# Kernel optimization log

Hardware: AMD Instinct MI355X
Metric: run time of the kernel (lower is better)

## Reference

```python
import jax, jax.numpy as jnp
import numpy as np
import math

HIDDEN = 2048
N_HEADS = 32
N_KV_HEADS = 8
HEAD_DIM = HIDDEN // N_HEADS
KV_REPEATS = N_HEADS // N_KV_HEADS
INTER = 4 * HIDDEN
EPS = 1e-5
B, Q, K = 2, 2048, 2048


def setup_inputs() -> dict:
    key = jax.random.key(0)
    ks = jax.random.split(key, 10)
    s = 0.02
    return {
        "hidden_states": jax.random.normal(ks[0], (B, Q, HIDDEN), jnp.float32),
        "key_states": jax.random.normal(ks[1], (B, K, N_KV_HEADS, HEAD_DIM), jnp.float32),
        "value_states": jax.random.normal(ks[2], (B, K, N_KV_HEADS, HEAD_DIM), jnp.float32),
        "gmu_memory": jnp.zeros((1,), jnp.float32),
        "w_ln1": jnp.ones((HIDDEN,), jnp.float32),
        "w_ln2": jnp.ones((HIDDEN,), jnp.float32),
        "w_q": jax.random.normal(ks[3], (N_HEADS * HEAD_DIM, HIDDEN), jnp.float32) * s,
        "w_o": jax.random.normal(ks[4], (HIDDEN, N_HEADS * HEAD_DIM), jnp.float32) * s,
        "w_gate": jax.random.normal(ks[5], (INTER, HIDDEN), jnp.float32) * s,
        "w_up": jax.random.normal(ks[6], (INTER, HIDDEN), jnp.float32) * s,
        "w_down": jax.random.normal(ks[7], (HIDDEN, INTER), jnp.float32) * s,
        "cu_seqlens_q": jnp.array([0, 1024, 2048], jnp.int32),
        "cu_seqlens_k": jnp.array([0, 1024, 2048], jnp.int32),
    }


def _rms_norm(x, w, eps=EPS):
    var = jnp.mean(jnp.square(x), axis=-1, keepdims=True)
    return (x * jax.lax.rsqrt(var + eps)) * w


def _segment_ids(cu, length):
    # position p belongs to segment i iff cu[i] <= p < cu[i+1]
    return jnp.searchsorted(cu[1:], jnp.arange(length), side="right")


def _attn_mask(q_len, k_len, cu_q, cu_k, causal=True, window_size=None):
    seg_q = _segment_ids(cu_q, q_len)  # [Q]
    seg_k = _segment_ids(cu_k, k_len)  # [K]
    mask = seg_q[:, None] == seg_k[None, :]
    if causal:
        q_pos = jnp.arange(q_len)[:, None]
        k_pos = jnp.arange(k_len)[None, :]
        offset = max(k_len - q_len, 0)
        mask = mask & (k_pos <= q_pos + offset)
    if window_size is not None and window_size > 0:
        q_pos = jnp.arange(q_len)[:, None] + max(k_len - q_len, 0)
        k_pos = jnp.arange(k_len)[None, :]
        mask = mask & (q_pos - k_pos < window_size)
    return mask  # [Q, K] bool


def reference(hidden_states, key_states, value_states, gmu_memory,
              w_ln1, w_ln2, w_q, w_o, w_gate, w_up, w_down,
              cu_seqlens_q, cu_seqlens_k):
    b, q_len, _ = hidden_states.shape
    residual = hidden_states
    normed = _rms_norm(hidden_states, w_ln1)

    # --- cross attention (shared KV, GQA) ---
    q = (normed @ w_q.T).reshape(b, q_len, N_HEADS, HEAD_DIM)
    k = jnp.repeat(key_states, KV_REPEATS, axis=2)    # [B,K,H,hd]
    v = jnp.repeat(value_states, KV_REPEATS, axis=2)  # [B,K,H,hd]
    k_len = k.shape[1]

    scores = jnp.einsum("bqhd,bkhd->bhqk", q, k) / math.sqrt(HEAD_DIM)
    mask = _attn_mask(q_len, k_len, cu_seqlens_q, cu_seqlens_k, causal=True)
    neg = jnp.finfo(scores.dtype).min
    scores = jnp.where(mask[None, None, :, :], scores, neg)
    probs = jax.nn.softmax(scores.astype(jnp.float32), axis=-1).astype(q.dtype)
    attn = jnp.einsum("bhqk,bkhd->bqhd", probs, v).reshape(b, q_len, -1)
    mixed = attn @ w_o.T

    hidden = residual + mixed

    # --- Llama MLP: down(silu(gate(x)) * up(x)) ---
    normed2 = _rms_norm(hidden, w_ln2)
    mlp = (jax.nn.silu(normed2 @ w_gate.T) * (normed2 @ w_up.T)) @ w_down.T
    return hidden + mlp
```

## Files before the change

### kernel.cpp

```cpp
#include <hip/hip_runtime.h>

typedef __bf16 bf16_t;
typedef bf16_t bf16x8 __attribute__((ext_vector_type(8)));
typedef float floatx4 __attribute__((ext_vector_type(4)));

#define HIDDEN 2048
#define NHEADS 32
#define NKV 8
#define HD 64
#define INTER 8192
#define SEQQ 2048
#define SEQK 2048
#define NBATCH 2
#define NEGBIG (-3.0e38f)

__device__ __forceinline__ floatx4 mfma16(bf16x8 a, bf16x8 b, floatx4 c) {
  return __builtin_amdgcn_mfma_f32_16x16x32_bf16(a, b, c, 0, 0, 0);
}

__device__ __forceinline__ uint4 pack8(const float* __restrict__ p) {
  float4 f0 = *(const float4*)p;
  float4 f1 = *(const float4*)(p + 4);
  union { uint4 u; bf16_t e[8]; } r;
  r.e[0] = (bf16_t)f0.x; r.e[1] = (bf16_t)f0.y; r.e[2] = (bf16_t)f0.z; r.e[3] = (bf16_t)f0.w;
  r.e[4] = (bf16_t)f1.x; r.e[5] = (bf16_t)f1.y; r.e[6] = (bf16_t)f1.z; r.e[7] = (bf16_t)f1.w;
  return r.u;
}

__global__ __launch_bounds__(256) void cvt_kernel(const float* __restrict__ src,
                                                  bf16_t* __restrict__ dst, int n8) {
  const int stride = gridDim.x * 256;
  for (int i = blockIdx.x * 256 + threadIdx.x; i < n8; i += stride)
    *(uint4*)(dst + (size_t)i * 8) = pack8(src + (size_t)i * 8);
}

__global__ __launch_bounds__(256) void rmsnorm_kernel(const float* __restrict__ x,
                                                      const float* __restrict__ w,
                                                      bf16_t* __restrict__ y) {
  const int row = blockIdx.x;
  const int tid = threadIdx.x;
  const float* xr = x + (size_t)row * HIDDEN + tid * 8;
  float4 x0 = *(const float4*)xr;
  float4 x1 = *(const float4*)(xr + 4);
  float xf[8] = {x0.x, x0.y, x0.z, x0.w, x1.x, x1.y, x1.z, x1.w};
  float ss = 0.f;
#pragma unroll
  for (int j = 0; j < 8; ++j) ss += xf[j] * xf[j];
#pragma unroll
  for (int off = 32; off >= 1; off >>= 1) ss += __shfl_xor(ss, off);
  __shared__ float red[4];
  if ((tid & 63) == 0) red[tid >> 6] = ss;
  __syncthreads();
  float tot = red[0] + red[1] + red[2] + red[3];
  float rs = 1.0f / sqrtf(tot / (float)HIDDEN + 1e-5f);
  const float* wr = w + tid * 8;
  float4 w0 = *(const float4*)wr;
  float4 w1 = *(const float4*)(wr + 4);
  float wf[8] = {w0.x, w0.y, w0.z, w0.w, w1.x, w1.y, w1.z, w1.w};
  bf16x8 ov;
#pragma unroll
  for (int j = 0; j < 8; ++j) ov[j] = (bf16_t)(xf[j] * rs * wf[j]);
  *(bf16x8*)(y + (size_t)row * HIDDEN + tid * 8) = ov;
}

template <int ROWS>
__device__ __forceinline__ void stage_tile(bf16_t* lds, const bf16_t* src, int ldK) {
  const int tid = (int)threadIdx.x;
  const int wid = tid >> 6;
  const int row0 = tid >> 3;
  const int scol = (((tid & 7) ^ (row0 & 7)) * 8);
#pragma unroll
  for (int i = 0; i < ROWS / 32; ++i) {
    const bf16_t* g = src + (size_t)(i * 32 + row0) * ldK + scol;
    __builtin_amdgcn_global_load_lds(
        (const __attribute__((address_space(1))) void*)g,
        (__attribute__((address_space(3))) void*)(lds + i * 2048 + wid * 512), 16, 0, 0);
  }
}

__device__ __forceinline__ bf16x8 ldfrag(const bf16_t* lds, int row, int kslot) {
  return *(const bf16x8*)(lds + row * 64 + ((kslot ^ (row & 7)) * 8));
}

template <int EPI, typename CT>
__global__ __launch_bounds__(256) void gemm_bt16(const bf16_t* __restrict__ A,
                                                 const bf16_t* __restrict__ W,
                                                 const float* __restrict__ resid,
                                                 CT* __restrict__ C, int Kd, int N) {
  const int m0 = blockIdx.y * 128, n0 = blockIdx.x * 128;
  const int tid = threadIdx.x;
  const int wid = tid >> 6, lane = tid & 63, quad = lane >> 4, l15 = lane & 15;
  const int wr = wid >> 1, wc = wid & 1;
  __shared__ __align__(16) bf16_t Asm[128 * 64];
  __shared__ __align__(16) bf16_t Bsm[128 * 64];
  floatx4 acc[4][4];
  floatx4 zero = {0.f, 0.f, 0.f, 0.f};
#pragma unroll
  for (int mi = 0; mi < 4; ++mi)
#pragma unroll
    for (int ni = 0; ni < 4; ++ni) acc[mi][ni] = zero;

  const bf16_t* Ab = A + (size_t)m0 * Kd;
  const bf16_t* Wb = W + (size_t)n0 * Kd;

  for (int kt = 0; kt < Kd; kt += 64) {
    __syncthreads();
    stage_tile<128>(Asm, Ab + kt, Kd);
    stage_tile<128>(Bsm, Wb + kt, Kd);
    __syncthreads();
#pragma unroll
    for (int kk = 0; kk < 2; ++kk) {
      const int ks = kk * 4 + quad;
      bf16x8 af[4], bfr[4];
#pragma unroll
      for (int mi = 0; mi < 4; ++mi) af[mi] = ldfrag(Asm, wr * 64 + mi * 16 + l15, ks);
#pragma unroll
      for (int ni = 0; ni < 4; ++ni) bfr[ni] = ldfrag(Bsm, wc * 64 + ni * 16 + l15, ks);
#pragma unroll
      for (int mi = 0; mi < 4; ++mi)
#pragma unroll
        for (int ni = 0; ni < 4; ++ni) acc[mi][ni] = mfma16(af[mi], bfr[ni], acc[mi][ni]);
    }
  }

#pragma unroll
  for (int mi = 0; mi < 4; ++mi) {
    const int mb = m0 + wr * 64 + mi * 16 + quad * 4;
#pragma unroll
    for (int ni = 0; ni < 4; ++ni) {
      const int n = n0 + wc * 64 + ni * 16 + l15;
      floatx4 v = acc[mi][ni];
#pragma unroll
      for (int r = 0; r < 4; ++r) {
        size_t idx = (size_t)(mb + r) * N + n;
        float val = v[r];
        if (EPI == 1) val += resid[idx];
        C[idx] = (CT)val;
      }
    }
  }
}

__global__ __launch_bounds__(256) void gateup16(const bf16_t* __restrict__ A,
                                                const bf16_t* __restrict__ Wg,
                                                const bf16_t* __restrict__ Wu,
                                                bf16_t* __restrict__ C, int Kd, int N) {
  const int m0 = blockIdx.y * 128, n0 = blockIdx.x * 64;
  const int tid = threadIdx.x;
  const int wid = tid >> 6, lane = tid & 63, quad = lane >> 4, l15 = lane & 15;
  const int wr = wid >> 1, wc = wid & 1;
  __shared__ __align__(16) bf16_t Asm[128 * 64];
  __shared__ __align__(16) bf16_t Gsm[64 * 64];
  __shared__ __align__(16) bf16_t Usm[64 * 64];
  floatx4 accg[4][2], accu[4][2];
  floatx4 zero = {0.f, 0.f, 0.f, 0.f};
#pragma unroll
  for (int mi = 0; mi < 4; ++mi)
#pragma unroll
    for (int ni = 0; ni < 2; ++ni) { accg[mi][ni] = zero; accu[mi][ni] = zero; }

  const bf16_t* Ab = A + (size_t)m0 * Kd;
  const bf16_t* Gb = Wg + (size_t)n0 * Kd;
  const bf16_t* Ub = Wu + (size_t)n0 * Kd;

  for (int kt = 0; kt < Kd; kt += 64) {
    __syncthreads();
    stage_tile<128>(Asm, Ab + kt, Kd);
    stage_tile<64>(Gsm, Gb + kt, Kd);
    stage_tile<64>(Usm, Ub + kt, Kd);
    __syncthreads();
#pragma unroll
    for (int kk = 0; kk < 2; ++kk) {
      const int ks = kk * 4 + quad;
      bf16x8 af[4];
#pragma unroll
      for (int mi = 0; mi < 4; ++mi) af[mi] = ldfrag(Asm, wr * 64 + mi * 16 + l15, ks);
#pragma unroll
      for (int ni = 0; ni < 2; ++ni) {
        bf16x8 bg = ldfrag(Gsm, wc * 32 + ni * 16 + l15, ks);
        bf16x8 bu = ldfrag(Usm, wc * 32 + ni * 16 + l15, ks);
#pragma unroll
        for (int mi = 0; mi < 4; ++mi) {
          accg[mi][ni] = mfma16(af[mi], bg, accg[mi][ni]);
          accu[mi][ni] = mfma16(af[mi], bu, accu[mi][ni]);
        }
      }
    }
  }

#pragma unroll
  for (int mi = 0; mi < 4; ++mi) {
    const int mb = m0 + wr * 64 + mi * 16 + quad * 4;
#pragma unroll
    for (int ni = 0; ni < 2; ++ni) {
      const int n = n0 + wc * 32 + ni * 16 + l15;
#pragma unroll
      for (int r = 0; r < 4; ++r) {
        float g = accg[mi][ni][r];
        float u = accu[mi][ni][r];
        float act = g / (1.f + __expf(-g)) * u;
        C[(size_t)(mb + r) * N + n] = (bf16_t)act;
      }
    }
  }
}

__global__ __launch_bounds__(256) void attn16(const bf16_t* __restrict__ qbuf,
                                              const bf16_t* __restrict__ kbuf,
                                              const bf16_t* __restrict__ vbuf,
                                              const int* __restrict__ cuq,
                                              const int* __restrict__ cuk,
                                              bf16_t* __restrict__ obuf) {
  const int qt = blockIdx.x, h = blockIdx.y, b = blockIdx.z;
  const int hk = h >> 2;
  const int tid = threadIdx.x;
  const int wid = tid >> 6, lane = tid & 63, quad = lane >> 4, l15 = lane & 15;
  __shared__ __align__(16) bf16_t Kt[64 * 72];
  __shared__ __align__(16) bf16_t Vt[64 * 72];
  __shared__ __align__(16) bf16_t Pt[64 * 72];
  const int cq1 = cuq[1], ck1 = cuk[1];

  const int qrow_a = qt * 64 + wid * 16 + l15;
  const bf16_t* qp = qbuf + ((size_t)(b * SEQQ + qrow_a)) * HIDDEN + h * HD;
  bf16x8 qf0 = *(const bf16x8*)(qp + quad * 8);
  bf16x8 qf1 = *(const bf16x8*)(qp + 32 + quad * 8);

  floatx4 Of[4];
  floatx4 zero = {0.f, 0.f, 0.f, 0.f};
#pragma unroll
  for (int df = 0; df < 4; ++df) Of[df] = zero;
  float m_r[4], l_r[4];
#pragma unroll
  for (int r = 0; r < 4; ++r) { m_r[r] = -1e30f; l_r[r] = 0.f; }
  const int q_row0 = qt * 64 + wid * 16 + quad * 4;
  int seg_q[4];
#pragma unroll
  for (int r = 0; r < 4; ++r) seg_q[r] = (q_row0 + r >= cq1) ? 1 : 0;
  const bool blk_seg1 = (qt * 64 >= cq1);

  const int stag_row = tid >> 3;
  const int stag_c = (tid & 7) * 8;
  const int kt_start = blk_seg1 ? (ck1 >> 6) : 0;

  for (int kt = kt_start; kt <= qt; ++kt) {
    __syncthreads();
#pragma unroll
    for (int i = 0; i < 2; ++i) {
      const int row = stag_row + i * 32;
      const size_t goff = ((size_t)((b * SEQK + kt * 64 + row) * NKV + hk)) * HD + stag_c;
      *(uint4*)&Kt[row * 72 + stag_c] = *(const uint4*)(kbuf + goff);
      bf16x8 vv = *(const bf16x8*)(vbuf + goff);
#pragma unroll
      for (int j = 0; j < 8; ++j) Vt[(stag_c + j) * 72 + row] = vv[j];
    }
    __syncthreads();

    floatx4 sf[4];
#pragma unroll
    for (int nf = 0; nf < 4; ++nf) {
      bf16x8 kf0 = *(const bf16x8*)&Kt[(nf * 16 + l15) * 72 + quad * 8];
      bf16x8 kf1 = *(const bf16x8*)&Kt[(nf * 16 + l15) * 72 + 32 + quad * 8];
      floatx4 a = zero;
      a = mfma16(qf0, kf0, a);
      a = mfma16(qf1, kf1, a);
      sf[nf] = a;
    }

    float tmax[4];
#pragma unroll
    for (int r = 0; r < 4; ++r) tmax[r] = NEGBIG;
#pragma unroll
    for (int nf = 0; nf < 4; ++nf) {
      const int kg = kt * 64 + nf * 16 + l15;
#pragma unroll
      for (int r = 0; r < 4; ++r) {
        const int qg = q_row0 + r;
        const int sk = (kg >= ck1) ? 1 : 0;
        float s = sf[nf][r] * 0.125f;
        bool ok = (kg <= qg) && (sk == seg_q[r]);
        s = ok ? s : NEGBIG;
        sf[nf][r] = s;
        tmax[r] = fmaxf(tmax[r], s);
      }
    }
#pragma unroll
    for (int r = 0; r < 4; ++r) {
#pragma unroll
      for (int off = 1; off <= 8; off <<= 1) tmax[r] = fmaxf(tmax[r], __shfl_xor(tmax[r], off));
    }
    float alpha[4], rsum[4];
#pragma unroll
    for (int r = 0; r < 4; ++r) {
      float mn = fmaxf(m_r[r], tmax[r]);
      alpha[r] = __expf(m_r[r] - mn);
      m_r[r] = mn;
      rsum[r] = 0.f;
    }
#pragma unroll
    for (int nf = 0; nf < 4; ++nf) {
#pragma unroll
      for (int r = 0; r < 4; ++r) {
        float p = __expf(sf[nf][r] - m_r[r]);
        rsum[r] += p;
        Pt[(wid * 16 + quad * 4 + r) * 72 + nf * 16 + l15] = (bf16_t)p;
      }
    }
#pragma unroll
    for (int r = 0; r < 4; ++r) {
#pragma unroll
      for (int off = 1; off <= 8; off <<= 1) rsum[r] += __shfl_xor(rsum[r], off);
      l_r[r] = alpha[r] * l_r[r] + rsum[r];
    }
#pragma unroll
    for (int df = 0; df < 4; ++df) {
#pragma unroll
      for (int r = 0; r < 4; ++r) Of[df][r] *= alpha[r];
    }
#pragma unroll
    for (int kk = 0; kk < 2; ++kk) {
      bf16x8 pf = *(const bf16x8*)&Pt[(wid * 16 + l15) * 72 + kk * 32 + quad * 8];
#pragma unroll
      for (int df = 0; df < 4; ++df) {
        bf16x8 vf = *(const bf16x8*)&Vt[(df * 16 + l15) * 72 + kk * 32 + quad * 8];
        Of[df] = mfma16(pf, vf, Of[df]);
      }
    }
  }

  float inv[4];
#pragma unroll
  for (int r = 0; r < 4; ++r) inv[r] = (l_r[r] > 0.f) ? 1.f / l_r[r] : 0.f;
#pragma unroll
  for (int df = 0; df < 4; ++df) {
#pragma unroll
    for (int r = 0; r < 4; ++r) {
      obuf[((size_t)(b * SEQQ + q_row0 + r)) * HIDDEN + h * HD + df * 16 + l15] =
          (bf16_t)(Of[df][r] * inv[r]);
    }
  }
}

template <int EPI, typename CT>
__global__ __launch_bounds__(256) void gemm_bt(const bf16_t* __restrict__ A,
                                               const float* __restrict__ W,
                                               const float* __restrict__ resid,
                                               CT* __restrict__ C,
                                               int Kd, int N) {
  const int m0 = blockIdx.y * 128, n0 = blockIdx.x * 128;
  const int tid = threadIdx.x;
  const int wid = tid >> 6, lane = tid & 63, quad = lane >> 4, l15 = lane & 15;
  const int wr = wid >> 1, wc = wid & 1;
  __shared__ __align__(16) bf16_t Asm[128 * 40];
  __shared__ __align__(16) bf16_t Bsm[128 * 40];
  floatx4 acc[4][4];
  floatx4 zero = {0.f, 0.f, 0.f, 0.f};
#pragma unroll
  for (int mi = 0; mi < 4; ++mi)
#pragma unroll
    for (int ni = 0; ni < 4; ++ni) acc[mi][ni] = zero;

  const int r0 = tid >> 2;
  const int c0 = (tid & 3) * 8;

  for (int kt = 0; kt < Kd; kt += 32) {
    __syncthreads();
    uint4 a0 = *(const uint4*)(A + (size_t)(m0 + r0) * Kd + kt + c0);
    uint4 a1 = *(const uint4*)(A + (size_t)(m0 + r0 + 64) * Kd + kt + c0);
    uint4 b0 = pack8(W + (size_t)(n0 + r0) * Kd + kt + c0);
    uint4 b1 = pack8(W + (size_t)(n0 + r0 + 64) * Kd + kt + c0);
    *(uint4*)&Asm[r0 * 40 + c0] = a0;
    *(uint4*)&Asm[(r0 + 64) * 40 + c0] = a1;
    *(uint4*)&Bsm[r0 * 40 + c0] = b0;
    *(uint4*)&Bsm[(r0 + 64) * 40 + c0] = b1;
    __syncthreads();
    bf16x8 af[4], bfrag[4];
#pragma unroll
    for (int mi = 0; mi < 4; ++mi)
      af[mi] = *(const bf16x8*)&Asm[(wr * 64 + mi * 16 + l15) * 40 + quad * 8];
#pragma unroll
    for (int ni = 0; ni < 4; ++ni)
      bfrag[ni] = *(const bf16x8*)&Bsm[(wc * 64 + ni * 16 + l15) * 40 + quad * 8];
#pragma unroll
    for (int mi = 0; mi < 4; ++mi)
#pragma unroll
      for (int ni = 0; ni < 4; ++ni)
        acc[mi][ni] = mfma16(af[mi], bfrag[ni], acc[mi][ni]);
  }

#pragma unroll
  for (int mi = 0; mi < 4; ++mi) {
    const int mb = m0 + wr * 64 + mi * 16 + quad * 4;
#pragma unroll
    for (int ni = 0; ni < 4; ++ni) {
      const int n = n0 + wc * 64 + ni * 16 + l15;
      floatx4 v = acc[mi][ni];
#pragma unroll
      for (int r = 0; r < 4; ++r) {
        size_t idx = (size_t)(mb + r) * N + n;
        float val = v[r];
        if (EPI == 1) val += resid[idx];
        C[idx] = (CT)val;
      }
    }
  }
}

__global__ __launch_bounds__(256) void gemm_gateup(const bf16_t* __restrict__ A,
                                                   const float* __restrict__ Wg,
                                                   const float* __restrict__ Wu,
                                                   bf16_t* __restrict__ C,
                                                   int Kd, int N) {
  const int m0 = blockIdx.y * 128, n0 = blockIdx.x * 128;
  const int tid = threadIdx.x;
  const int wid = tid >> 6, lane = tid & 63, quad = lane >> 4, l15 = lane & 15;
  const int wr = wid >> 1, wc = wid & 1;
  __shared__ __align__(16) bf16_t Asm[128 * 40];
  __shared__ __align__(16) bf16_t Gsm[128 * 40];
  __shared__ __align__(16) bf16_t Usm[128 * 40];
  floatx4 accg[4][4], accu[4][4];
  floatx4 zero = {0.f, 0.f, 0.f, 0.f};
#pragma unroll
  for (int mi = 0; mi < 4; ++mi)
#pragma unroll
    for (int ni = 0; ni < 4; ++ni) { accg[mi][ni] = zero; accu[mi][ni] = zero; }

  const int r0 = tid >> 2;
  const int c0 = (tid & 3) * 8;

  for (int kt = 0; kt < Kd; kt += 32) {
    __syncthreads();
    uint4 a0 = *(const uint4*)(A + (size_t)(m0 + r0) * Kd + kt + c0);
    uint4 a1 = *(const uint4*)(A + (size_t)(m0 + r0 + 64) * Kd + kt + c0);
    uint4 g0 = pack8(Wg + (size_t)(n0 + r0) * Kd + kt + c0);
    uint4 g1 = pack8(Wg + (size_t)(n0 + r0 + 64) * Kd + kt + c0);
    uint4 u0 = pack8(Wu + (size_t)(n0 + r0) * Kd + kt + c0);
    uint4 u1 = pack8(Wu + (size_t)(n0 + r0 + 64) * Kd + kt + c0);
    *(uint4*)&Asm[r0 * 40 + c0] = a0;
    *(uint4*)&Asm[(r0 + 64) * 40 + c0] = a1;
    *(uint4*)&Gsm[r0 * 40 + c0] = g0;
    *(uint4*)&Gsm[(r0 + 64) * 40 + c0] = g1;
    *(uint4*)&Usm[r0 * 40 + c0] = u0;
    *(uint4*)&Usm[(r0 + 64) * 40 + c0] = u1;
    __syncthreads();
    bf16x8 af[4];
#pragma unroll
    for (int mi = 0; mi < 4; ++mi)
      af[mi] = *(const bf16x8*)&Asm[(wr * 64 + mi * 16 + l15) * 40 + quad * 8];
#pragma unroll
    for (int ni = 0; ni < 4; ++ni) {
      bf16x8 bg = *(const bf16x8*)&Gsm[(wc * 64 + ni * 16 + l15) * 40 + quad * 8];
      bf16x8 bu = *(const bf16x8*)&Usm[(wc * 64 + ni * 16 + l15) * 40 + quad * 8];
#pragma unroll
      for (int mi = 0; mi < 4; ++mi) {
        accg[mi][ni] = mfma16(af[mi], bg, accg[mi][ni]);
        accu[mi][ni] = mfma16(af[mi], bu, accu[mi][ni]);
      }
    }
  }

#pragma unroll
  for (int mi = 0; mi < 4; ++mi) {
    const int mb = m0 + wr * 64 + mi * 16 + quad * 4;
#pragma unroll
    for (int ni = 0; ni < 4; ++ni) {
      const int n = n0 + wc * 64 + ni * 16 + l15;
#pragma unroll
      for (int r = 0; r < 4; ++r) {
        float g = accg[mi][ni][r];
        float u = accu[mi][ni][r];
        float act = g / (1.f + __expf(-g)) * u;
        C[(size_t)(mb + r) * N + n] = (bf16_t)act;
      }
    }
  }
}

__global__ __launch_bounds__(256) void attn_kernel(const bf16_t* __restrict__ qbuf,
                                                   const float* __restrict__ kbuf,
                                                   const float* __restrict__ vbuf,
                                                   const int* __restrict__ cuq,
                                                   const int* __restrict__ cuk,
                                                   bf16_t* __restrict__ obuf) {
  const int qt = blockIdx.x, h = blockIdx.y, b = blockIdx.z;
  const int hk = h >> 2;
  const int tid = threadIdx.x;
  const int wid = tid >> 6, lane = tid & 63, quad = lane >> 4, l15 = lane & 15;
  __shared__ __align__(16) bf16_t Kt[64 * 72];
  __shared__ __align__(16) bf16_t Vt[64 * 72];
  __shared__ __align__(16) bf16_t Pt[64 * 72];
  const int cq1 = cuq[1], ck1 = cuk[1];

  const int qrow_a = qt * 64 + wid * 16 + l15;
  const bf16_t* qp = qbuf + ((size_t)(b * SEQQ + qrow_a)) * HIDDEN + h * HD;
  bf16x8 qf0 = *(const bf16x8*)(qp + quad * 8);
  bf16x8 qf1 = *(const bf16x8*)(qp + 32 + quad * 8);

  floatx4 Of[4];
  floatx4 zero = {0.f, 0.f, 0.f, 0.f};
#pragma unroll
  for (int df = 0; df < 4; ++df) Of[df] = zero;
  float m_r[4], l_r[4];
#pragma unroll
  for (int r = 0; r < 4; ++r) { m_r[r] = -1e30f; l_r[r] = 0.f; }
  const int q_row0 = qt * 64 + wid * 16 + quad * 4;
  int seg_q[4];
#pragma unroll
  for (int r = 0; r < 4; ++r) seg_q[r] = (q_row0 + r >= cq1) ? 1 : 0;
  const bool blk_seg1 = (qt * 64 >= cq1);

  const int stag_row = tid >> 3;
  const int stag_c = (tid & 7) * 8;
  const int kt_start = blk_seg1 ? (ck1 >> 6) : 0;

  for (int kt = kt_start; kt <= qt; ++kt) {
    __syncthreads();
#pragma unroll
    for (int i = 0; i < 2; ++i) {
      const int row = stag_row + i * 32;
      const size_t goff = ((size_t)((b * SEQK + kt * 64 + row) * NKV + hk)) * HD + stag_c;
      uint4 kv = pack8(kbuf + goff);
      *(uint4*)&Kt[row * 72 + stag_c] = kv;
      union { uint4 u; bf16_t e[8]; } vv;
      vv.u = pack8(vbuf + goff);
#pragma unroll
      for (int j = 0; j < 8; ++j) Vt[(stag_c + j) * 72 + row] = vv.e[j];
    }
    __syncthreads();

    floatx4 sf[4];
#pragma unroll
    for (int nf = 0; nf < 4; ++nf) {
      bf16x8 kf0 = *(const bf16x8*)&Kt[(nf * 16 + l15) * 72 + quad * 8];
      bf16x8 kf1 = *(const bf16x8*)&Kt[(nf * 16 + l15) * 72 + 32 + quad * 8];
      floatx4 a = zero;
      a = mfma16(qf0, kf0, a);
      a = mfma16(qf1, kf1, a);
      sf[nf] = a;
    }

    float tmax[4];
#pragma unroll
    for (int r = 0; r < 4; ++r) tmax[r] = NEGBIG;
#pragma unroll
    for (int nf = 0; nf < 4; ++nf) {
      const int kg = kt * 64 + nf * 16 + l15;
#pragma unroll
      for (int r = 0; r < 4; ++r) {
        const int qg = q_row0 + r;
        const int sk = (kg >= ck1) ? 1 : 0;
        float s = sf[nf][r] * 0.125f;
        bool ok = (kg <= qg) && (sk == seg_q[r]);
        s = ok ? s : NEGBIG;
        sf[nf][r] = s;
        tmax[r] = fmaxf(tmax[r], s);
      }
    }
#pragma unroll
    for (int r = 0; r < 4; ++r) {
#pragma unroll
      for (int off = 1; off <= 8; off <<= 1) tmax[r] = fmaxf(tmax[r], __shfl_xor(tmax[r], off));
    }
    float alpha[4], rsum[4];
#pragma unroll
    for (int r = 0; r < 4; ++r) {
      float mn = fmaxf(m_r[r], tmax[r]);
      alpha[r] = __expf(m_r[r] - mn);
      m_r[r] = mn;
      rsum[r] = 0.f;
    }
#pragma unroll
    for (int nf = 0; nf < 4; ++nf) {
#pragma unroll
      for (int r = 0; r < 4; ++r) {
        float p = __expf(sf[nf][r] - m_r[r]);
        rsum[r] += p;
        Pt[(wid * 16 + quad * 4 + r) * 72 + nf * 16 + l15] = (bf16_t)p;
      }
    }
#pragma unroll
    for (int r = 0; r < 4; ++r) {
#pragma unroll
      for (int off = 1; off <= 8; off <<= 1) rsum[r] += __shfl_xor(rsum[r], off);
      l_r[r] = alpha[r] * l_r[r] + rsum[r];
    }
#pragma unroll
    for (int df = 0; df < 4; ++df) {
#pragma unroll
      for (int r = 0; r < 4; ++r) Of[df][r] *= alpha[r];
    }
#pragma unroll
    for (int kk = 0; kk < 2; ++kk) {
      bf16x8 pf = *(const bf16x8*)&Pt[(wid * 16 + l15) * 72 + kk * 32 + quad * 8];
#pragma unroll
      for (int df = 0; df < 4; ++df) {
        bf16x8 vf = *(const bf16x8*)&Vt[(df * 16 + l15) * 72 + kk * 32 + quad * 8];
        Of[df] = mfma16(pf, vf, Of[df]);
      }
    }
  }

  float inv[4];
#pragma unroll
  for (int r = 0; r < 4; ++r) inv[r] = (l_r[r] > 0.f) ? 1.f / l_r[r] : 0.f;
#pragma unroll
  for (int df = 0; df < 4; ++df) {
#pragma unroll
    for (int r = 0; r < 4; ++r) {
      obuf[((size_t)(b * SEQQ + q_row0 + r)) * HIDDEN + h * HD + df * 16 + l15] =
          (bf16_t)(Of[df][r] * inv[r]);
    }
  }
}

static inline int cvt_grid(int n8) {
  int g = (n8 + 255) / 256;
  return g > 2048 ? 2048 : g;
}

extern "C" void kernel_launch(void* const* d_in, const int* in_sizes, int n_in,
                              void* d_out, int out_size, void* d_ws, size_t ws_size,
                              hipStream_t stream) {
  const float* x    = (const float*)d_in[0];
  const float* kst  = (const float*)d_in[1];
  const float* vst  = (const float*)d_in[2];
  const float* wln1 = (const float*)d_in[4];
  const float* wln2 = (const float*)d_in[5];
  const float* wq   = (const float*)d_in[6];
  const float* wo   = (const float*)d_in[7];
  const float* wg   = (const float*)d_in[8];
  const float* wu   = (const float*)d_in[9];
  const float* wd   = (const float*)d_in[10];
  const int* cuq    = (const int*)d_in[11];
  const int* cuk    = (const int*)d_in[12];
  float* out = (float*)d_out;

  const size_t MB = 1024ull * 1024ull;
  char* ws = (char*)d_ws;
  const bool full = ws_size >= 200 * MB;
  const bool conv = ws_size >= 168 * MB;

  if (conv) {
    bf16_t* bufA = (bf16_t*)ws;
    bf16_t* bufB = (bf16_t*)(ws + 16 * MB);
    char* p = ws + 16 * MB + (full ? 64 : 32) * MB;
    bf16_t* wq16 = (bf16_t*)p; p += 8 * MB;
    bf16_t* wo16 = (bf16_t*)p; p += 8 * MB;
    bf16_t* wg16 = (bf16_t*)p; p += 32 * MB;
    bf16_t* wu16 = (bf16_t*)p; p += 32 * MB;
    bf16_t* wd16 = (bf16_t*)p; p += 32 * MB;
    bf16_t* k16  = (bf16_t*)p; p += 4 * MB;
    bf16_t* v16  = (bf16_t*)p;

    const int n8_qo = 2048 * 2048 / 8;
    const int n8_gud = 8192 * 2048 / 8;
    const int n8_kv = NBATCH * SEQK * NKV * HD / 8;
    cvt_kernel<<<cvt_grid(n8_qo), 256, 0, stream>>>(wq, wq16, n8_qo);
    cvt_kernel<<<cvt_grid(n8_qo), 256, 0, stream>>>(wo, wo16, n8_qo);
    cvt_kernel<<<cvt_grid(n8_gud), 256, 0, stream>>>(wg, wg16, n8_gud);
    cvt_kernel<<<cvt_grid(n8_gud), 256, 0, stream>>>(wu, wu16, n8_gud);
    cvt_kernel<<<cvt_grid(n8_gud), 256, 0, stream>>>(wd, wd16, n8_gud);
    cvt_kernel<<<cvt_grid(n8_kv), 256, 0, stream>>>(kst, k16, n8_kv);
    cvt_kernel<<<cvt_grid(n8_kv), 256, 0, stream>>>(vst, v16, n8_kv);

    rmsnorm_kernel<<<4096, 256, 0, stream>>>(x, wln1, bufA);
    gemm_bt16<0, bf16_t><<<dim3(16, 32), 256, 0, stream>>>(bufA, wq16, nullptr, bufB, 2048, 2048);
    attn16<<<dim3(32, 32, 2), 256, 0, stream>>>(bufB, k16, v16, cuq, cuk, bufA);
    gemm_bt16<1, float><<<dim3(16, 32), 256, 0, stream>>>(bufA, wo16, x, out, 2048, 2048);
    rmsnorm_kernel<<<4096, 256, 0, stream>>>(out, wln2, bufA);
    const int nch = full ? 1 : 2;
    const int mch = 4096 / nch;
    for (int c = 0; c < nch; ++c) {
      const size_t off = (size_t)c * mch;
      gateup16<<<dim3(128, mch / 128), 256, 0, stream>>>(bufA + off * HIDDEN, wg16, wu16,
                                                         bufB, 2048, 8192);
      gemm_bt16<1, float><<<dim3(16, mch / 128), 256, 0, stream>>>(bufB, wd16, out + off * HIDDEN,
                                                                   out + off * HIDDEN, 8192, 2048);
    }
  } else {
    bf16_t* bufA = (bf16_t*)ws;
    bf16_t* bufB = (bf16_t*)(ws + 16 * MB);
    rmsnorm_kernel<<<4096, 256, 0, stream>>>(x, wln1, bufA);
    gemm_bt<0, bf16_t><<<dim3(16, 32), 256, 0, stream>>>(bufA, wq, nullptr, bufB, 2048, 2048);
    attn_kernel<<<dim3(32, 32, 2), 256, 0, stream>>>(bufB, kst, vst, cuq, cuk, bufA);
    gemm_bt<1, float><<<dim3(16, 32), 256, 0, stream>>>(bufA, wo, x, out, 2048, 2048);
    rmsnorm_kernel<<<4096, 256, 0, stream>>>(out, wln2, bufA);
    for (int c = 0; c < 2; ++c) {
      const size_t off = (size_t)c * 2048;
      gemm_gateup<<<dim3(64, 16), 256, 0, stream>>>(bufA + off * HIDDEN, wg, wu, bufB, 2048, 8192);
      gemm_bt<1, float><<<dim3(16, 16), 256, 0, stream>>>(bufB, wd, out + off * HIDDEN,
                                                          out + off * HIDDEN, 8192, 2048);
    }
  }
}
```

Measured before the change: 1.023 ms.

## Triple-buffer GEMM tiles with 256-row blocks, grid swizzle, and MFMA priority

Replaces the single-buffered 128x128 bf16 GEMM and gate/up kernels with 512-thread, 256-row-tile versions. Global-to-LDS loads now run through a three-stage buffer ring, with prefetch two tiles ahead interleaved between the MFMA half-steps, and explicit vmcnt waits replacing the double barriers. It also adds a workgroup ID swizzle for L2 locality and raises wave priority around MFMA blocks. This targets load latency and barrier stalls, at the cost of much larger LDS use (about 144KB and 120KB), which limits occupancy to one block per CU, and fewer blocks in the grid.

```diff
diff --git a/kernel.cpp b/kernel.cpp
--- a/kernel.cpp
+++ b/kernel.cpp
@@ -63,19 +63,14 @@
   *(bf16x8*)(y + (size_t)row * HIDDEN + tid * 8) = ov;
 }
 
-template <int ROWS>
-__device__ __forceinline__ void stage_tile(bf16_t* lds, const bf16_t* src, int ldK) {
+
+__device__ __forceinline__ void stg512(bf16_t* lds, const bf16_t* src, int ldK, int i) {
   const int tid = (int)threadIdx.x;
-  const int wid = tid >> 6;
-  const int row0 = tid >> 3;
-  const int scol = (((tid & 7) ^ (row0 & 7)) * 8);
-#pragma unroll
-  for (int i = 0; i < ROWS / 32; ++i) {
-    const bf16_t* g = src + (size_t)(i * 32 + row0) * ldK + scol;
-    __builtin_amdgcn_global_load_lds(
-        (const __attribute__((address_space(1))) void*)g,
-        (__attribute__((address_space(3))) void*)(lds + i * 2048 + wid * 512), 16, 0, 0);
-  }
+  const int row = i * 64 + (tid >> 3);
+  const int col = (((tid & 7) ^ (row & 7)) * 8);
+  __builtin_amdgcn_global_load_lds(
+      (const __attribute__((address_space(1))) void*)(src + (size_t)row * ldK + col),
+      (__attribute__((address_space(3))) void*)(lds + i * 4096 + (tid >> 6) * 512), 16, 0, 0);
 }
 
 __device__ __forceinline__ bf16x8 ldfrag(const bf16_t* lds, int row, int kslot) {
@@ -83,16 +78,22 @@
 }
 
 template <int EPI, typename CT>
-__global__ __launch_bounds__(256) void gemm_bt16(const bf16_t* __restrict__ A,
-                                                 const bf16_t* __restrict__ W,
-                                                 const float* __restrict__ resid,
-                                                 CT* __restrict__ C, int Kd, int N) {
-  const int m0 = blockIdx.y * 128, n0 = blockIdx.x * 128;
+__global__ __launch_bounds__(512) void gemm256(const bf16_t* __restrict__ A,
+                                               const bf16_t* __restrict__ W,
+                                               const float* __restrict__ resid,
+                                               CT* __restrict__ C, int Kd, int N) {
+  __shared__ __align__(16) bf16_t AS[3][256 * 64];
+  __shared__ __align__(16) bf16_t BS[3][128 * 64];
   const int tid = threadIdx.x;
   const int wid = tid >> 6, lane = tid & 63, quad = lane >> 4, l15 = lane & 15;
   const int wr = wid >> 1, wc = wid & 1;
-  __shared__ __align__(16) bf16_t Asm[128 * 64];
-  __shared__ __align__(16) bf16_t Bsm[128 * 64];
+  const int nbx = gridDim.x, nby = gridDim.y;
+  const int nwg = nbx * nby;
+  const int wgid = (int)blockIdx.x * nby + (int)blockIdx.y;
+  const int swz = (wgid & 7) * (nwg >> 3) + (wgid >> 3);
+  const int bx = swz / nby, by = swz - bx * nby;
+  const int m0 = by * 256, n0 = bx * 128;
+
   floatx4 acc[4][4];
   floatx4 zero = {0.f, 0.f, 0.f, 0.f};
 #pragma unroll
@@ -102,24 +103,59 @@
 
   const bf16_t* Ab = A + (size_t)m0 * Kd;
   const bf16_t* Wb = W + (size_t)n0 * Kd;
-
-  for (int kt = 0; kt < Kd; kt += 64) {
-    __syncthreads();
-    stage_tile<128>(Asm, Ab + kt, Kd);
-    stage_tile<128>(Bsm, Wb + kt, Kd);
-    __syncthreads();
-#pragma unroll
-    for (int kk = 0; kk < 2; ++kk) {
-      const int ks = kk * 4 + quad;
+  const int NT = Kd >> 6;
+
+#pragma unroll
+  for (int i = 0; i < 4; ++i) stg512(AS[0], Ab, Kd, i);
+#pragma unroll
+  for (int i = 0; i < 2; ++i) stg512(BS[0], Wb, Kd, i);
+#pragma unroll
+  for (int i = 0; i < 4; ++i) stg512(AS[1], Ab + 64, Kd, i);
+#pragma unroll
+  for (int i = 0; i < 2; ++i) stg512(BS[1], Wb + 64, Kd, i);
+
+  for (int t = 0; t < NT; ++t) {
+    const int b = t % 3;
+    const bf16_t* As = &AS[b][0];
+    const bf16_t* Bs = &BS[b][0];
+    if (t < NT - 1)
+      asm volatile("s_waitcnt vmcnt(6)\n\ts_barrier" ::: "memory");
+    else
+      asm volatile("s_waitcnt vmcnt(0)\n\ts_barrier" ::: "memory");
+    const int t2 = t + 2;
+    const bool pf = (t2 < NT);
+    bf16_t* As2 = &AS[t2 % 3][0];
+    bf16_t* Bs2 = &BS[t2 % 3][0];
+    const bf16_t* Ag = Ab + t2 * 64;
+    const bf16_t* Bg = Wb + t2 * 64;
+
+    if (pf) { stg512(As2, Ag, Kd, 0); stg512(As2, Ag, Kd, 1); stg512(Bs2, Bg, Kd, 0); }
+    {
       bf16x8 af[4], bfr[4];
 #pragma unroll
-      for (int mi = 0; mi < 4; ++mi) af[mi] = ldfrag(Asm, wr * 64 + mi * 16 + l15, ks);
-#pragma unroll
-      for (int ni = 0; ni < 4; ++ni) bfr[ni] = ldfrag(Bsm, wc * 64 + ni * 16 + l15, ks);
+      for (int mi = 0; mi < 4; ++mi) af[mi] = ldfrag(As, wr * 64 + mi * 16 + l15, quad);
+#pragma unroll
+      for (int ni = 0; ni < 4; ++ni) bfr[ni] = ldfrag(Bs, wc * 64 + ni * 16 + l15, quad);
+      __builtin_amdgcn_s_setprio(1);
 #pragma unroll
       for (int mi = 0; mi < 4; ++mi)
 #pragma unroll
         for (int ni = 0; ni < 4; ++ni) acc[mi][ni] = mfma16(af[mi], bfr[ni], acc[mi][ni]);
+      __builtin_amdgcn_s_setprio(0);
+    }
+    if (pf) { stg512(As2, Ag, Kd, 2); stg512(As2, Ag, Kd, 3); stg512(Bs2, Bg, Kd, 1); }
+    {
+      bf16x8 af[4], bfr[4];
+#pragma unroll
+      for (int mi = 0; mi < 4; ++mi) af[mi] = ldfrag(As, wr * 64 + mi * 16 + l15, 4 + quad);
+#pragma unroll
+      for (int ni = 0; ni < 4; ++ni) bfr[ni] = ldfrag(Bs, wc * 64 + ni * 16 + l15, 4 + quad);
+      __builtin_amdgcn_s_setprio(1);
+#pragma unroll
+      for (int mi = 0; mi < 4; ++mi)
+#pragma unroll
+        for (int ni = 0; ni < 4; ++ni) acc[mi][ni] = mfma16(af[mi], bfr[ni], acc[mi][ni]);
+      __builtin_amdgcn_s_setprio(0);
     }
   }
 
@@ -141,17 +177,23 @@
   }
 }
 
-__global__ __launch_bounds__(256) void gateup16(const bf16_t* __restrict__ A,
-                                                const bf16_t* __restrict__ Wg,
-                                                const bf16_t* __restrict__ Wu,
-                                                bf16_t* __restrict__ C, int Kd, int N) {
-  const int m0 = blockIdx.y * 128, n0 = blockIdx.x * 64;
+__global__ __launch_bounds__(512) void gateup256(const bf16_t* __restrict__ A,
+                                                 const bf16_t* __restrict__ Wg,
+                                                 const bf16_t* __restrict__ Wu,
+                                                 bf16_t* __restrict__ C, int Kd, int N) {
+  __shared__ __align__(16) bf16_t AS[3][256 * 64];
+  __shared__ __align__(16) bf16_t GS[3][64 * 64];
+  __shared__ __align__(16) bf16_t US[3][64 * 64];
   const int tid = threadIdx.x;
   const int wid = tid >> 6, lane = tid & 63, quad = lane >> 4, l15 = lane & 15;
   const int wr = wid >> 1, wc = wid & 1;
-  __shared__ __align__(16) bf16_t Asm[128 * 64];
-  __shared__ __align__(16) bf16_t Gsm[64 * 64];
-  __shared__ __align__(16) bf16_t Usm[64 * 64];
+  const int nbx = gridDim.x, nby = gridDim.y;
+  const int nwg = nbx * nby;
+  const int wgid = (int)blockIdx.x * nby + (int)blockIdx.y;
+  const int swz = (wgid & 7) * (nwg >> 3) + (wgid >> 3);
+  const int bx = swz / nby, by = swz - bx * nby;
+  const int m0 = by * 256, n0 = bx * 64;
+
   floatx4 accg[4][2], accu[4][2];
   floatx4 zero = {0.f, 0.f, 0.f, 0.f};
 #pragma unroll
@@ -162,29 +204,74 @@
   const bf16_t* Ab = A + (size_t)m0 * Kd;
   const bf16_t* Gb = Wg + (size_t)n0 * Kd;
   const bf16_t* Ub = Wu + (size_t)n0 * Kd;
-
-  for (int kt = 0; kt < Kd; kt += 64) {
-    __syncthreads();
-    stage_tile<128>(Asm, Ab + kt, Kd);
-    stage_tile<64>(Gsm, Gb + kt, Kd);
-    stage_tile<64>(Usm, Ub + kt, Kd);
-    __syncthreads();
-#pragma unroll
-    for (int kk = 0; kk < 2; ++kk) {
-      const int ks = kk * 4 + quad;
-      bf16x8 af[4];
-#pragma unroll
-      for (int mi = 0; mi < 4; ++mi) af[mi] = ldfrag(Asm, wr * 64 + mi * 16 + l15, ks);
+  const int NT = Kd >> 6;
+
+#pragma unroll
+  for (int i = 0; i < 4; ++i) stg512(AS[0], Ab, Kd, i);
+  stg512(GS[0], Gb, Kd, 0);
+  stg512(US[0], Ub, Kd, 0);
+#pragma unroll
+  for (int i = 0; i < 4; ++i) stg512(AS[1], Ab + 64, Kd, i);
+  stg512(GS[1], Gb + 64, Kd, 0);
+  stg512(US[1], Ub + 64, Kd, 0);
+
+  for (int t = 0; t < NT; ++t) {
+    const int b = t % 3;
+    const bf16_t* As = &AS[b][0];
+    const bf16_t* Gs = &GS[b][0];
+    const bf16_t* Us = &US[b][0];
+    if (t < NT - 1)
+      asm volatile("s_waitcnt vmcnt(6)\n\ts_barrier" ::: "memory");
+    else
+      asm volatile("s_waitcnt vmcnt(0)\n\ts_barrier" ::: "memory");
+    const int t2 = t + 2;
+    const bool pf = (t2 < NT);
+    bf16_t* As2 = &AS[t2 % 3][0];
+    bf16_t* Gs2 = &GS[t2 % 3][0];
+    bf16_t* Us2 = &US[t2 % 3][0];
+    const bf16_t* Ag = Ab + t2 * 64;
+    const bf16_t* Gg = Gb + t2 * 64;
+    const bf16_t* Ug = Ub + t2 * 64;
+
+    if (pf) { stg512(As2, Ag, Kd, 0); stg512(As2, Ag, Kd, 1); stg512(Gs2, Gg, Kd, 0); }
+    {
+      bf16x8 af[4], gf[2], uf[2];
+#pragma unroll
+      for (int mi = 0; mi < 4; ++mi) af[mi] = ldfrag(As, wr * 64 + mi * 16 + l15, quad);
 #pragma unroll
       for (int ni = 0; ni < 2; ++ni) {
-        bf16x8 bg = ldfrag(Gsm, wc * 32 + ni * 16 + l15, ks);
-        bf16x8 bu = ldfrag(Usm, wc * 32 + ni * 16 + l15, ks);
-#pragma unroll
-        for (int mi = 0; mi < 4; ++mi) {
-          accg[mi][ni] = mfma16(af[mi], bg, accg[mi][ni]);
-          accu[mi][ni] = mfma16(af[mi], bu, accu[mi][ni]);
+        gf[ni] = ldfrag(Gs, wc * 32 + ni * 16 + l15, quad);
+        uf[ni] = ldfrag(Us, wc * 32 + ni * 16 + l15, quad);
+      }
+      __builtin_amdgcn_s_setprio(1);
+#pragma unroll
+      for (int mi = 0; mi < 4; ++mi)
+#pragma unroll
+        for (int ni = 0; ni < 2; ++ni) {
+          accg[mi][ni] = mfma16(af[mi], gf[ni], accg[mi][ni]);
+          accu[mi][ni] = mfma16(af[mi], uf[ni], accu[mi][ni]);
         }
-      }
+      __builtin_amdgcn_s_setprio(0);
+    }
+    if (pf) { stg512(As2, Ag, Kd, 2); stg512(As2, Ag, Kd, 3); stg512(Us2, Ug, Kd, 0); }
+    {
+      bf16x8 af[4], gf[2], uf[2];
+#pragma unroll
+      for (int mi = 0; mi < 4; ++mi) af[mi] = ldfrag(As, wr * 64 + mi * 16 + l15, 4 + quad);
+#pragma unroll
+      for (int ni = 0; ni < 2; ++ni) {
+        gf[ni] = ldfrag(Gs, wc * 32 + ni * 16 + l15, 4 + quad);
+        uf[ni] = ldfrag(Us, wc * 32 + ni * 16 + l15, 4 + quad);
+      }
+      __builtin_amdgcn_s_setprio(1);
+#pragma unroll
+      for (int mi = 0; mi < 4; ++mi)
+#pragma unroll
+        for (int ni = 0; ni < 2; ++ni) {
+          accg[mi][ni] = mfma16(af[mi], gf[ni], accg[mi][ni]);
+          accu[mi][ni] = mfma16(af[mi], uf[ni], accu[mi][ni]);
+        }
+      __builtin_amdgcn_s_setprio(0);
     }
   }
 
@@ -663,18 +750,18 @@
     cvt_kernel<<<cvt_grid(n8_kv), 256, 0, stream>>>(vst, v16, n8_kv);
 
     rmsnorm_kernel<<<4096, 256, 0, stream>>>(x, wln1, bufA);
-    gemm_bt16<0, bf16_t><<<dim3(16, 32), 256, 0, stream>>>(bufA, wq16, nullptr, bufB, 2048, 2048);
+    gemm256<0, bf16_t><<<dim3(16, 16), 512, 0, stream>>>(bufA, wq16, nullptr, bufB, 2048, 2048);
     attn16<<<dim3(32, 32, 2), 256, 0, stream>>>(bufB, k16, v16, cuq, cuk, bufA);
-    gemm_bt16<1, float><<<dim3(16, 32), 256, 0, stream>>>(bufA, wo16, x, out, 2048, 2048);
+    gemm256<1, float><<<dim3(16, 16), 512, 0, stream>>>(bufA, wo16, x, out, 2048, 2048);
     rmsnorm_kernel<<<4096, 256, 0, stream>>>(out, wln2, bufA);
     const int nch = full ? 1 : 2;
     const int mch = 4096 / nch;
     for (int c = 0; c < nch; ++c) {
       const size_t off = (size_t)c * mch;
-      gateup16<<<dim3(128, mch / 128), 256, 0, stream>>>(bufA + off * HIDDEN, wg16, wu16,
-                                                         bufB, 2048, 8192);
-      gemm_bt16<1, float><<<dim3(16, mch / 128), 256, 0, stream>>>(bufB, wd16, out + off * HIDDEN,
-                                                                   out + off * HIDDEN, 8192, 2048);
+      gateup256<<<dim3(128, mch / 256), 512, 0, stream>>>(bufA + off * HIDDEN, wg16, wu16,
+                                                          bufB, 2048, 8192);
+      gemm256<1, float><<<dim3(16, mch / 256), 512, 0, stream>>>(bufB, wd16, out + off * HIDDEN,
+                                                                 out + off * HIDDEN, 8192, 2048);
     }
   } else {
     bf16_t* bufA = (bf16_t*)ws;
```

Result: slower. 1.228 ms (+20.0%).

## Restructure attention to share KV tiles across head pairs with double-buffered V

Applied to the files above, without the earlier changes.

Replaces the per-head attention kernel with a version where each block handles two query heads sharing one KV head, each wave doing 32 query rows for one head. K fragments are now loaded straight from global into registers, with no LDS staging. V is prefetched into registers and written to a double-buffered LDS tile, which cuts the syncs per iteration from two to one. This halves the grid and raises reuse of KV loads, at the cost of more registers per thread and redundant global K reads across waves.

```diff
diff --git a/kernel.cpp b/kernel.cpp
--- a/kernel.cpp
+++ b/kernel.cpp
@@ -205,137 +205,188 @@
   }
 }
 
-__global__ __launch_bounds__(256) void attn16(const bf16_t* __restrict__ qbuf,
-                                              const bf16_t* __restrict__ kbuf,
-                                              const bf16_t* __restrict__ vbuf,
-                                              const int* __restrict__ cuq,
-                                              const int* __restrict__ cuk,
-                                              bf16_t* __restrict__ obuf) {
-  const int qt = blockIdx.x, h = blockIdx.y, b = blockIdx.z;
-  const int hk = h >> 2;
+__global__ __launch_bounds__(256) void attn_gqa(const bf16_t* __restrict__ qbuf,
+                                                const bf16_t* __restrict__ kbuf,
+                                                const bf16_t* __restrict__ vbuf,
+                                                const int* __restrict__ cuq,
+                                                const int* __restrict__ cuk,
+                                                bf16_t* __restrict__ obuf) {
+  const int qt = blockIdx.x, hg = blockIdx.y, b = blockIdx.z;
+  const int hk = hg >> 1;
   const int tid = threadIdx.x;
   const int wid = tid >> 6, lane = tid & 63, quad = lane >> 4, l15 = lane & 15;
-  __shared__ __align__(16) bf16_t Kt[64 * 72];
-  __shared__ __align__(16) bf16_t Vt[64 * 72];
-  __shared__ __align__(16) bf16_t Pt[64 * 72];
+  const int h = hg * 2 + (wid >> 1);
+  const int qh = wid & 1;
+  __shared__ __align__(16) bf16_t Vt[2][64 * 72];
+  __shared__ __align__(16) bf16_t Pt[4 * 32 * 72];
   const int cq1 = cuq[1], ck1 = cuk[1];
 
-  const int qrow_a = qt * 64 + wid * 16 + l15;
-  const bf16_t* qp = qbuf + ((size_t)(b * SEQQ + qrow_a)) * HIDDEN + h * HD;
-  bf16x8 qf0 = *(const bf16x8*)(qp + quad * 8);
-  bf16x8 qf1 = *(const bf16x8*)(qp + 32 + quad * 8);
-
-  floatx4 Of[4];
+  bf16x8 qf[2][2];
+#pragma unroll
+  for (int mi = 0; mi < 2; ++mi) {
+    const int qr = qt * 64 + qh * 32 + mi * 16 + l15;
+    const bf16_t* qp = qbuf + ((size_t)(b * SEQQ + qr)) * HIDDEN + h * HD;
+    qf[mi][0] = *(const bf16x8*)(qp + quad * 8);
+    qf[mi][1] = *(const bf16x8*)(qp + 32 + quad * 8);
+  }
+
+  floatx4 Of[2][4];
   floatx4 zero = {0.f, 0.f, 0.f, 0.f};
 #pragma unroll
-  for (int df = 0; df < 4; ++df) Of[df] = zero;
-  float m_r[4], l_r[4];
-#pragma unroll
-  for (int r = 0; r < 4; ++r) { m_r[r] = -1e30f; l_r[r] = 0.f; }
-  const int q_row0 = qt * 64 + wid * 16 + quad * 4;
-  int seg_q[4];
-#pragma unroll
-  for (int r = 0; r < 4; ++r) seg_q[r] = (q_row0 + r >= cq1) ? 1 : 0;
+  for (int mi = 0; mi < 2; ++mi)
+#pragma unroll
+    for (int df = 0; df < 4; ++df) Of[mi][df] = zero;
+  float m_r[2][4], l_r[2][4];
+#pragma unroll
+  for (int mi = 0; mi < 2; ++mi)
+#pragma unroll
+    for (int r = 0; r < 4; ++r) { m_r[mi][r] = -1e30f; l_r[mi][r] = 0.f; }
+
   const bool blk_seg1 = (qt * 64 >= cq1);
-
-  const int stag_row = tid >> 3;
-  const int stag_c = (tid & 7) * 8;
   const int kt_start = blk_seg1 ? (ck1 >> 6) : 0;
 
+  const int vrow = tid >> 3;
+  const int vc = (tid & 7) * 8;
+
+#pragma unroll
+  for (int i = 0; i < 2; ++i) {
+    const int row = vrow + i * 32;
+    const size_t goff = ((size_t)((b * SEQK + kt_start * 64 + row) * NKV + hk)) * HD + vc;
+    bf16x8 vv = *(const bf16x8*)(vbuf + goff);
+#pragma unroll
+    for (int j = 0; j < 8; ++j) Vt[kt_start & 1][(vc + j) * 72 + row] = vv[j];
+  }
+
   for (int kt = kt_start; kt <= qt; ++kt) {
-    __syncthreads();
-#pragma unroll
-    for (int i = 0; i < 2; ++i) {
-      const int row = stag_row + i * 32;
-      const size_t goff = ((size_t)((b * SEQK + kt * 64 + row) * NKV + hk)) * HD + stag_c;
-      *(uint4*)&Kt[row * 72 + stag_c] = *(const uint4*)(kbuf + goff);
-      bf16x8 vv = *(const bf16x8*)(vbuf + goff);
-#pragma unroll
-      for (int j = 0; j < 8; ++j) Vt[(stag_c + j) * 72 + row] = vv[j];
-    }
-    __syncthreads();
-
-    floatx4 sf[4];
+    const int p = kt & 1;
+    const bool hn = (kt < qt);
+    bf16x8 vvn[2];
+    if (hn) {
+#pragma unroll
+      for (int i = 0; i < 2; ++i) {
+        const int row = vrow + i * 32;
+        const size_t goff = ((size_t)((b * SEQK + (kt + 1) * 64 + row) * NKV + hk)) * HD + vc;
+        vvn[i] = *(const bf16x8*)(vbuf + goff);
+      }
+    }
+    bf16x8 kf[4][2];
 #pragma unroll
     for (int nf = 0; nf < 4; ++nf) {
-      bf16x8 kf0 = *(const bf16x8*)&Kt[(nf * 16 + l15) * 72 + quad * 8];
-      bf16x8 kf1 = *(const bf16x8*)&Kt[(nf * 16 + l15) * 72 + 32 + quad * 8];
-      floatx4 a = zero;
-      a = mfma16(qf0, kf0, a);
-      a = mfma16(qf1, kf1, a);
-      sf[nf] = a;
-    }
-
-    float tmax[4];
-#pragma unroll
-    for (int r = 0; r < 4; ++r) tmax[r] = NEGBIG;
-#pragma unroll
-    for (int nf = 0; nf < 4; ++nf) {
-      const int kg = kt * 64 + nf * 16 + l15;
-#pragma unroll
-      for (int r = 0; r < 4; ++r) {
-        const int qg = q_row0 + r;
+      const int krow = kt * 64 + nf * 16 + l15;
+      const bf16_t* kp = kbuf + ((size_t)((b * SEQK + krow) * NKV + hk)) * HD;
+      kf[nf][0] = *(const bf16x8*)(kp + quad * 8);
+      kf[nf][1] = *(const bf16x8*)(kp + 32 + quad * 8);
+    }
+    floatx4 sf[2][4];
+#pragma unroll
+    for (int mi = 0; mi < 2; ++mi)
+#pragma unroll
+      for (int nf = 0; nf < 4; ++nf) {
+        floatx4 a = zero;
+        a = mfma16(qf[mi][0], kf[nf][0], a);
+        a = mfma16(qf[mi][1], kf[nf][1], a);
+        sf[mi][nf] = a;
+      }
+
+    float tmax[2][4];
+#pragma unroll
+    for (int mi = 0; mi < 2; ++mi) {
+      const int q0 = qt * 64 + qh * 32 + mi * 16 + quad * 4;
+#pragma unroll
+      for (int r = 0; r < 4; ++r) tmax[mi][r] = NEGBIG;
+#pragma unroll
+      for (int nf = 0; nf < 4; ++nf) {
+        const int kg = kt * 64 + nf * 16 + l15;
         const int sk = (kg >= ck1) ? 1 : 0;
-        float s = sf[nf][r] * 0.125f;
-        bool ok = (kg <= qg) && (sk == seg_q[r]);
-        s = ok ? s : NEGBIG;
-        sf[nf][r] = s;
-        tmax[r] = fmaxf(tmax[r], s);
-      }
-    }
+#pragma unroll
+        for (int r = 0; r < 4; ++r) {
+          const int qg = q0 + r;
+          const int sq = (qg >= cq1) ? 1 : 0;
+          float s = sf[mi][nf][r] * 0.125f;
+          bool ok = (kg <= qg) && (sk == sq);
+          s = ok ? s : NEGBIG;
+          sf[mi][nf][r] = s;
+          tmax[mi][r] = fmaxf(tmax[mi][r], s);
+        }
+      }
+#pragma unroll
+      for (int r = 0; r < 4; ++r) {
+#pragma unroll
+        for (int off = 1; off <= 8; off <<= 1)
+          tmax[mi][r] = fmaxf(tmax[mi][r], __shfl_xor(tmax[mi][r], off));
+      }
+    }
+    float alpha[2][4], rsum[2][4];
+#pragma unroll
+    for (int mi = 0; mi < 2; ++mi)
+#pragma unroll
+      for (int r = 0; r < 4; ++r) {
+        float mn = fmaxf(m_r[mi][r], tmax[mi][r]);
+        alpha[mi][r] = __expf(m_r[mi][r] - mn);
+        m_r[mi][r] = mn;
+        rsum[mi][r] = 0.f;
+      }
+#pragma unroll
+    for (int mi = 0; mi < 2; ++mi)
+#pragma unroll
+      for (int nf = 0; nf < 4; ++nf)
+#pragma unroll
+        for (int r = 0; r < 4; ++r) {
+          float pv = __expf(sf[mi][nf][r] - m_r[mi][r]);
+          rsum[mi][r] += pv;
+          Pt[(wid * 32 + mi * 16 + quad * 4 + r) * 72 + nf * 16 + l15] = (bf16_t)pv;
+        }
+#pragma unroll
+    for (int mi = 0; mi < 2; ++mi)
+#pragma unroll
+      for (int r = 0; r < 4; ++r) {
+#pragma unroll
+        for (int off = 1; off <= 8; off <<= 1) rsum[mi][r] += __shfl_xor(rsum[mi][r], off);
+        l_r[mi][r] = alpha[mi][r] * l_r[mi][r] + rsum[mi][r];
+      }
+#pragma unroll
+    for (int mi = 0; mi < 2; ++mi)
+#pragma unroll
+      for (int df = 0; df < 4; ++df)
+#pragma unroll
+        for (int r = 0; r < 4; ++r) Of[mi][df][r] *= alpha[mi][r];
+
+    __syncthreads();
+
+    if (hn) {
+#pragma unroll
+      for (int i = 0; i < 2; ++i) {
+        const int row = vrow + i * 32;
+#pragma unroll
+        for (int j = 0; j < 8; ++j) Vt[p ^ 1][(vc + j) * 72 + row] = vvn[i][j];
+      }
+    }
+
+#pragma unroll
+    for (int kk = 0; kk < 2; ++kk) {
+#pragma unroll
+      for (int mi = 0; mi < 2; ++mi) {
+        bf16x8 pfr = *(const bf16x8*)&Pt[(wid * 32 + mi * 16 + l15) * 72 + kk * 32 + quad * 8];
+#pragma unroll
+        for (int df = 0; df < 4; ++df) {
+          bf16x8 vfr = *(const bf16x8*)&Vt[p][(df * 16 + l15) * 72 + kk * 32 + quad * 8];
+          Of[mi][df] = mfma16(pfr, vfr, Of[mi][df]);
+        }
+      }
+    }
+  }
+
+#pragma unroll
+  for (int mi = 0; mi < 2; ++mi) {
+    const int q0 = qt * 64 + qh * 32 + mi * 16 + quad * 4;
 #pragma unroll
     for (int r = 0; r < 4; ++r) {
-#pragma unroll
-      for (int off = 1; off <= 8; off <<= 1) tmax[r] = fmaxf(tmax[r], __shfl_xor(tmax[r], off));
-    }
-    float alpha[4], rsum[4];
-#pragma unroll
-    for (int r = 0; r < 4; ++r) {
-      float mn = fmaxf(m_r[r], tmax[r]);
-      alpha[r] = __expf(m_r[r] - mn);
-      m_r[r] = mn;
-      rsum[r] = 0.f;
-    }
-#pragma unroll
-    for (int nf = 0; nf < 4; ++nf) {
-#pragma unroll
-      for (int r = 0; r < 4; ++r) {
-        float p = __expf(sf[nf][r] - m_r[r]);
-        rsum[r] += p;
-        Pt[(wid * 16 + quad * 4 + r) * 72 + nf * 16 + l15] = (bf16_t)p;
-      }
-    }
-#pragma unroll
-    for (int r = 0; r < 4; ++r) {
-#pragma unroll
-      for (int off = 1; off <= 8; off <<= 1) rsum[r] += __shfl_xor(rsum[r], off);
-      l_r[r] = alpha[r] * l_r[r] + rsum[r];
-    }
-#pragma unroll
-    for (int df = 0; df < 4; ++df) {
-#pragma unroll
-      for (int r = 0; r < 4; ++r) Of[df][r] *= alpha[r];
-    }
-#pragma unroll
-    for (int kk = 0; kk < 2; ++kk) {
-      bf16x8 pf = *(const bf16x8*)&Pt[(wid * 16 + l15) * 72 + kk * 32 + quad * 8];
+      float inv = (l_r[mi][r] > 0.f) ? 1.f / l_r[mi][r] : 0.f;
 #pragma unroll
       for (int df = 0; df < 4; ++df) {
-        bf16x8 vf = *(const bf16x8*)&Vt[(df * 16 + l15) * 72 + kk * 32 + quad * 8];
-        Of[df] = mfma16(pf, vf, Of[df]);
-      }
-    }
-  }
-
-  float inv[4];
-#pragma unroll
-  for (int r = 0; r < 4; ++r) inv[r] = (l_r[r] > 0.f) ? 1.f / l_r[r] : 0.f;
-#pragma unroll
-  for (int df = 0; df < 4; ++df) {
-#pragma unroll
-    for (int r = 0; r < 4; ++r) {
-      obuf[((size_t)(b * SEQQ + q_row0 + r)) * HIDDEN + h * HD + df * 16 + l15] =
-          (bf16_t)(Of[df][r] * inv[r]);
+        obuf[((size_t)(b * SEQQ + q0 + r)) * HIDDEN + h * HD + df * 16 + l15] =
+            (bf16_t)(Of[mi][df][r] * inv);
+      }
     }
   }
 }
@@ -664,7 +715,7 @@
 
     rmsnorm_kernel<<<4096, 256, 0, stream>>>(x, wln1, bufA);
     gemm_bt16<0, bf16_t><<<dim3(16, 32), 256, 0, stream>>>(bufA, wq16, nullptr, bufB, 2048, 2048);
-    attn16<<<dim3(32, 32, 2), 256, 0, stream>>>(bufB, k16, v16, cuq, cuk, bufA);
+    attn_gqa<<<dim3(32, 16, 2), 256, 0, stream>>>(bufB, k16, v16, cuq, cuk, bufA);
     gemm_bt16<1, float><<<dim3(16, 32), 256, 0, stream>>>(bufA, wo16, x, out, 2048, 2048);
     rmsnorm_kernel<<<4096, 256, 0, stream>>>(out, wln2, bufA);
     const int nch = full ? 1 : 2;
```

After: 1.012 ms. Within noise of the previous version (-1.1%).
